# Performance work log

Hardware: AMD Instinct MI355X
Metric: run time of the kernel (lower is better)

The kernel has to match this reference:

```python
import jax, jax.numpy as jnp
import numpy as np
from jax import lax

B, C, H, Wd = 8, 3, 256, 256
K = 32           # kernels
LAT = K * 8      # 256, latent dim
P = 7            # patch size
HALF = P // 2
S = 1024         # samples per image
PD = C * P * P   # 147
NEG = 0.01       # LeakyReLU slope
EPS = 1e-5


def setup_inputs() -> dict:
    key = jax.random.key(0)
    ks = jax.random.split(key, 20)
    x = jax.random.normal(ks[0], (B, C, H, Wd), dtype=jnp.float32)
    # patch centers must satisfy HALF <= c <= H-1-HALF (here [3, 252])
    anchors_hw = jax.random.randint(ks[1], (B, S, 2), HALF, H - HALF, dtype=jnp.int32)
    positives_hw = jax.random.randint(ks[2], (B, S, 2), HALF, H - HALF, dtype=jnp.int32)
    def w(k, shape, fan_in):
        return jax.random.normal(k, shape, dtype=jnp.float32) * (1.0 / np.sqrt(fan_in))
    inp = dict(x=x, anchors_hw=anchors_hw, positives_hw=positives_hw,
               w1=w(ks[3], (K, C, 3, 3), C * 9),        g1=jnp.ones((K,), jnp.float32),        b1=jnp.zeros((K,), jnp.float32),
               w2=w(ks[4], (2 * K, K, 3, 3), K * 9),    g2=jnp.ones((2 * K,), jnp.float32),    b2=jnp.zeros((2 * K,), jnp.float32),
               w3=w(ks[5], (4 * K, 2 * K, 3, 3), 2 * K * 9), g3=jnp.ones((4 * K,), jnp.float32), b3=jnp.zeros((4 * K,), jnp.float32),
               w4=w(ks[6], (8 * K, 4 * K, 3, 3), 4 * K * 9), g4=jnp.ones((8 * K,), jnp.float32), b4=jnp.zeros((8 * K,), jnp.float32),
               lin1_w=w(ks[7], (PD, LAT), LAT), lin1_b=jnp.zeros((PD,), jnp.float32),
               lin2_w=w(ks[8], (PD, PD), PD),   lin2_b=jnp.zeros((PD,), jnp.float32))
    return inp


def _conv(x, w):
    return lax.conv_general_dilated(x, w, (1, 1), 'SAME',
                                    dimension_numbers=('NCHW', 'OIHW', 'NCHW'))


def _bn(x, g, b):
    # training-mode BatchNorm2d: batch stats over (N,H,W)
    m = x.mean(axis=(0, 2, 3), keepdims=True)
    v = x.var(axis=(0, 2, 3), keepdims=True)
    return g[None, :, None, None] * (x - m) * lax.rsqrt(v + EPS) + b[None, :, None, None]


def _lrelu(x):
    return jnp.where(x >= 0, x, NEG * x)


def _forward(x, anchors_hw, positives_hw, w1, g1, b1, w2, g2, b2, w3, g3, b3,
             w4, g4, b4, lin1_w, lin1_b, lin2_w, lin2_b):
    feat = _lrelu(_bn(_conv(x, w1), g1, b1))
    feat = _lrelu(_bn(_conv(feat, w2), g2, b2))
    feat = _lrelu(_bn(_conv(feat, w3), g3, b3))
    feat = _lrelu(_bn(_conv(feat, w4), g4, b4))  # [B, LAT, H, W]

    fhwc = jnp.transpose(feat, (0, 2, 3, 1))  # [B,H,W,LAT]
    gather_pts = jax.vmap(lambda f, hw: f[hw[:, 0], hw[:, 1]])  # per-batch fancy gather
    W_anchors = gather_pts(fhwc, anchors_hw)      # [B,S,LAT]
    W_positives = gather_pts(fhwc, positives_hw)  # [B,S,LAT]

    def slice_one(img, hw):  # img [C,H,W], hw [2]
        return lax.dynamic_slice(img, (0, hw[0] - HALF, hw[1] - HALF), (C, P, P))
    patch_real = jax.vmap(jax.vmap(slice_one, in_axes=(None, 0)))(x, anchors_hw)  # [B,S,C,P,P]

    h = _lrelu(jnp.einsum('bsl,pl->bsp', W_anchors, lin1_w) + lin1_b)
    patch_recon = (jnp.einsum('bsp,qp->bsq', h, lin2_w) + lin2_b).reshape(x.shape[0], -1, C, P, P)
    return (feat, patch_real, patch_recon, W_anchors, W_positives)


def reference(x, anchors_hw, positives_hw, w1, g1, b1, w2, g2, b2, w3, g3, b3,
              w4, g4, b4, lin1_w, lin1_b, lin2_w, lin2_b):
    return _forward(x, anchors_hw, positives_hw, w1, g1, b1, w2, g2, b2,
                    w3, g3, b3, w4, g4, b4, lin1_w, lin1_b, lin2_w, lin2_b)
```

## Files before the change

### kernel.cpp

```cpp
#include <hip/hip_runtime.h>
#include <hip/hip_bf16.h>

typedef unsigned short u16;
typedef short bf16x8 __attribute__((ext_vector_type(8)));
typedef float f32x4 __attribute__((ext_vector_type(4)));
typedef unsigned short u16x8 __attribute__((ext_vector_type(8)));

#define PD 147

static const long OFF_PREAL = 134217728L;
static const long OFF_PRECON= 135421952L;
static const long OFF_WA    = 136626176L;
static const long OFF_WP    = 138723328L;

static const long RAW_SPLIT = 100663296L;

__device__ __forceinline__ float lrelu(float v){ return v >= 0.f ? v : 0.01f*v; }

__device__ __forceinline__ float bf2f(u16 u){
    union { unsigned int i; float f; } x; x.i = ((unsigned int)u) << 16; return x.f;
}
__device__ __forceinline__ u16 f2bf(float f){
    __hip_bfloat16 h = __float2bfloat16(f);
    return *reinterpret_cast<u16*>(&h);
}

__device__ __forceinline__ void gload16(const void* g, void* l){
    __builtin_amdgcn_global_load_lds((const __attribute__((address_space(1))) void*)g,
                                     (__attribute__((address_space(3))) void*)l, 16, 0, 0);
}

template<int CIN, int KOUT, bool SPLIT>
__global__ __launch_bounds__(512)
void conv_mfma(const u16* __restrict__ fin, const u16* __restrict__ wt,
               void* __restrict__ out_, u16* __restrict__ rawhi,
               float* __restrict__ part)
{
    constexpr int CC = CIN / 32;
    constexpr int NS3 = CC * 3;
    constexpr int NF = KOUT / 64;
    constexpr int ABYTES = 2 * 324 * 32 * 2;
    constexpr int BQ = 3 * KOUT * 4;
    constexpr int NB3 = (BQ + 511) / 512;
    constexpr int BBYTES = 2 * BQ * 16;
    constexpr int EPIB = 256 * KOUT * 2;
    constexpr int SB = (ABYTES + BBYTES) > EPIB ? (ABYTES + BBYTES) : EPIB;
    __shared__ __align__(16) char smem[SB];
    u16* As = (u16*)smem;
    u16* Bs = (u16*)(smem + ABYTES);

    const int tid = threadIdx.x;
    const int w = tid >> 6, lane = tid & 63;
    const int wm = w >> 2, wn = w & 3;
    const int tile = blockIdx.x;
    const int tx0 = (tile & 15) << 4, ty0 = (tile >> 4) << 4;
    const int b = blockIdx.y;
    const long pixbase = (long)b << 16;
    const int hi = lane >> 4;

    f32x4 acc[8][NF];
#pragma unroll
    for (int m = 0; m < 8; m++)
#pragma unroll
        for (int n = 0; n < NF; n++) acc[m][n] = (f32x4){0.f,0.f,0.f,0.f};

    for (int i = tid; i < ABYTES/16; i += 512)
        ((int4*)smem)[i] = make_int4(0,0,0,0);
    __syncthreads();

    auto stage_a_round = [&](int cc, int buf, int r){
        u16* dstbase = As + buf * (324*32);
        int q = r*512 + w*64 + lane;
        int pf = q >> 2, quarter = q & 3;
        int ly = pf / 18;
        int lx = pf - ly*18;
        int gy = ty0 + ly - 1, gx = tx0 + lx - 1;
        bool ok = (q < 1296) && ((unsigned)gy < 256u) && ((unsigned)gx < 256u);
        const u16* src = fin + ((pixbase + (gy<<8) + gx) * CIN + cc*32 + quarter*8);
        u16* dst = dstbase + (r*512 + w*64) * 8;
        if (ok) gload16(src, dst);
    };
    auto stage_b3 = [&](int s, int buf){
        int cc = s / 3, dyr = s - cc*3;
        int t0 = dyr * 3;
        u16* dstbase = Bs + buf * (BQ*16/2);
#pragma unroll
        for (int r = 0; r < NB3; ++r){
            int q = r*512 + w*64 + lane;
            int tl = q / (KOUT*4);
            int qq = q - tl*(KOUT*4);
            int k = qq >> 2, quarter = qq & 3;
            const u16* src = wt + (((long)(t0+tl)*KOUT + k) * CIN + cc*32 + quarter*8);
            u16* dst = dstbase + (r*512 + w*64) * 8;
            if (q < BQ) gload16(src, dst);
        }
    };

    stage_a_round(0, 0, 0); stage_a_round(0, 0, 1); stage_a_round(0, 0, 2);
    stage_b3(0, 0);
    __syncthreads();

#pragma unroll 1
    for (int s = 0; s < NS3; ++s){
        int cc = s / 3, dyr = s - cc*3;
        if (s + 1 < NS3) stage_b3(s + 1, (s + 1) & 1);
        if (cc + 1 < CC) stage_a_round(cc + 1, (cc + 1) & 1, dyr);

        const u16* Ab = As + (cc & 1) * (324*32);
        const u16* Bb = Bs + (s & 1) * (BQ*16/2);
#pragma unroll
        for (int t = 0; t < 3; ++t){
            bf16x8 av[8];
#pragma unroll
            for (int m = 0; m < 8; m++){
                int pf = (wm*8 + m + dyr)*18 + (lane & 15) + t;
                av[m] = *(const bf16x8*)(Ab + pf*32 + hi*8);
            }
            bf16x8 bv[NF];
#pragma unroll
            for (int n = 0; n < NF; n++){
                int ch = (wn*NF + n)*16 + (lane & 15);
                bv[n] = *(const bf16x8*)(Bb + (t*KOUT + ch)*32 + hi*8);
            }
#pragma unroll
            for (int m = 0; m < 8; m++)
#pragma unroll
                for (int n = 0; n < NF; n++)
                    acc[m][n] = __builtin_amdgcn_mfma_f32_16x16x32_bf16(av[m], bv[n], acc[m][n], 0, 0, 0);
        }
        __syncthreads();
    }

    {
        const int bid = blockIdx.y * 256 + blockIdx.x;
        const long slot = (long)bid * 2 + wm;
#pragma unroll
        for (int n = 0; n < NF; n++){
            float s = 0.f, s2 = 0.f;
#pragma unroll
            for (int m = 0; m < 8; m++)
#pragma unroll
                for (int j = 0; j < 4; j++){
                    float v = acc[m][n][j];
                    s += v; s2 += v*v;
                }
            s += __shfl_down(s, 32); s2 += __shfl_down(s2, 32);
            s += __shfl_down(s, 16); s2 += __shfl_down(s2, 16);
            if (lane < 16){
                int ch = (wn*NF + n)*16 + lane;
                long off = (slot*KOUT + ch)*2;
                part[off]   = s;
                part[off+1] = s2;
            }
        }
    }

    {
        u16* ep = (u16*)smem;
        u16* outh = (u16*)out_;
        if (SPLIT && b >= 6) outh = rawhi - RAW_SPLIT;
#pragma unroll
        for (int m = 0; m < 8; m++)
#pragma unroll
            for (int n = 0; n < NF; n++){
                int ch = (wn*NF + n)*16 + (lane&15);
#pragma unroll
                for (int j = 0; j < 4; j++){
                    int px = wm*128 + m*16 + (lane>>4)*4 + j;
                    ep[px*KOUT + ch] = f2bf(acc[m][n][j]);
                }
            }
        __syncthreads();
        const int n16 = 256*KOUT/8;
        const int upr = KOUT*2;
        for (int i = tid; i < n16; i += 512){
            int py = i / upr;
            int rem = i - py*upr;
            long ga = (pixbase + ((ty0+py)<<8) + tx0) * KOUT + (long)rem*8;
            *(int4*)(outh + ga) = *(int4*)(ep + (long)i*8);
        }
    }
}

__global__ __launch_bounds__(256)
void conv1_direct(const float* __restrict__ x, const float* __restrict__ w1, u16* __restrict__ f1)
{
    __shared__ float wl[864];
    const int t = threadIdx.x;
    for (int i = t; i < 864; i += 256) wl[i] = w1[i];
    __syncthreads();
    const int y = blockIdx.x, b = blockIdx.y;
    float acc[32];
#pragma unroll
    for (int k = 0; k < 32; k++) acc[k] = 0.f;
    const long ib = (long)b*3*65536;
    for (int c = 0; c < 3; c++){
#pragma unroll
        for (int dy = 0; dy < 3; dy++){
            int gy = y + dy - 1;
#pragma unroll
            for (int dx = 0; dx < 3; dx++){
                int gx = t + dx - 1;
                float v = 0.f;
                if ((unsigned)gy < 256u && (unsigned)gx < 256u)
                    v = x[ib + c*65536 + (gy<<8) + gx];
                const float* wp = &wl[c*9 + dy*3 + dx];
#pragma unroll
                for (int k = 0; k < 32; k++) acc[k] += v * wp[k*27];
            }
        }
    }
    u16 ub[32];
#pragma unroll
    for (int k = 0; k < 32; k++) ub[k] = f2bf(acc[k]);
    u16* dst = f1 + ((long)(b*65536 + (y<<8) + t)) * 32;
#pragma unroll
    for (int j = 0; j < 4; j++) *(int4*)(dst + j*8) = *(int4*)(ub + j*8);
}

__global__ __launch_bounds__(256)
void prep_w(const float* __restrict__ w, u16* __restrict__ wt, int K, int C)
{
    int i = blockIdx.x*256 + threadIdx.x;
    if (i >= 9*K*C) return;
    int c = i % C; int r = i / C; int k = r % K; int tap = r / K;
    wt[i] = f2bf(w[((long)k*C + c)*9 + tap]);
}

template<int C>
__global__ __launch_bounds__(256)
void bn_stats_nhwc(const u16* __restrict__ f, float* __restrict__ part)
{
    constexpr int CQ = C/4;
    constexpr int SUBS = 256/CQ;
    const int t = threadIdx.x;
    const int cq = t & (CQ-1);
    const int sub = t / CQ;
    const long rowbase = (long)blockIdx.x * 512;
    float s[4] = {0,0,0,0}, q2[4] = {0,0,0,0};
    for (int r = sub; r < 512; r += SUBS){
        ushort4 v = *(const ushort4*)(f + (rowbase + r)*C + cq*4);
        float x0 = bf2f(v.x), x1 = bf2f(v.y), x2 = bf2f(v.z), x3 = bf2f(v.w);
        s[0]+=x0; q2[0]+=x0*x0; s[1]+=x1; q2[1]+=x1*x1;
        s[2]+=x2; q2[2]+=x2*x2; s[3]+=x3; q2[3]+=x3*x3;
    }
    __shared__ float r0[256], r1[256];
    for (int j = 0; j < 4; j++){
        r0[t] = s[j]; r1[t] = q2[j];
        __syncthreads();
        for (int st = 128; st >= CQ; st >>= 1){
            if (t < st){ r0[t] += r0[t+st]; r1[t] += r1[t+st]; }
            __syncthreads();
        }
        if (t < CQ){
            part[((long)blockIdx.x * C + t*4 + j)*2]     = r0[t];
            part[((long)blockIdx.x * C + t*4 + j)*2 + 1] = r1[t];
        }
        __syncthreads();
    }
}

__global__ __launch_bounds__(256)
void bn_stats_final2(const float* __restrict__ part, const float* __restrict__ g,
                     const float* __restrict__ bb, int C, int NB2, float* __restrict__ ss)
{
    const int c = blockIdx.x, t = threadIdx.x;
    float s = 0.f, s2 = 0.f;
    for (int i = t; i < NB2; i += 256){
        s  += part[((long)i*C + c)*2];
        s2 += part[((long)i*C + c)*2 + 1];
    }
    __shared__ float r0[256], r1[256];
    r0[t] = s; r1[t] = s2;
    __syncthreads();
    for (int st = 128; st > 0; st >>= 1){
        if (t < st){ r0[t] += r0[t+st]; r1[t] += r1[t+st]; }
        __syncthreads();
    }
    if (t == 0){
        const float invN = 1.f/524288.f;
        float m = r0[0]*invN;
        float v = r1[0]*invN - m*m;
        float sc = g[c]/sqrtf(v + 1e-5f);
        ss[c] = sc; ss[C+c] = bb[c] - m*sc;
    }
}

template<int C>
__global__ __launch_bounds__(256)
void bn_apply(u16* __restrict__ f, const float* __restrict__ ss, long n8)
{
    long i = (long)blockIdx.x*256 + threadIdx.x;
    if (i >= n8) return;
    u16x8 v = *(u16x8*)(f + i*8);
    int c0 = (int)((i*8) & (C-1));
#pragma unroll
    for (int j = 0; j < 8; j++){
        float xx = bf2f(v[j]);
        xx = lrelu(ss[c0+j]*xx + ss[C+c0+j]);
        v[j] = f2bf(xx);
    }
    *(u16x8*)(f + i*8) = v;
}

__global__ __launch_bounds__(256)
void bn_expand_t(const u16* __restrict__ rawlo, const u16* __restrict__ rawhi,
                 const float* __restrict__ ss, float* __restrict__ feat, int b0)
{
    __shared__ u16 lds[64*258];
    const int bid = blockIdx.x;
    const int b = b0 + (bid >> 10);
    const int px0 = (bid & 1023) * 64;
    const long p0 = (((long)(b<<16) + px0)) << 8;
    const u16* src = (b < 6) ? (rawlo + p0) : (rawhi + (p0 - RAW_SPLIT));
    const int t = threadIdx.x;
#pragma unroll
    for (int it = 0; it < 8; ++it){
        int i = it*256 + t;
        int px = i >> 5, u = i & 31;
        *(u16x8*)&lds[px*258 + u*8] = *(const u16x8*)(src + (long)i*8);
    }
    __syncthreads();
#pragma unroll
    for (int it = 0; it < 16; ++it){
        int idx = it*256 + t;
        int ch = idx >> 4;
        int q  = idx & 15;
        const float sc = ss[ch], sh = ss[256 + ch];
        float4 o;
        o.x = lrelu(sc*bf2f(lds[(q*4+0)*258 + ch]) + sh);
        o.y = lrelu(sc*bf2f(lds[(q*4+1)*258 + ch]) + sh);
        o.z = lrelu(sc*bf2f(lds[(q*4+2)*258 + ch]) + sh);
        o.w = lrelu(sc*bf2f(lds[(q*4+3)*258 + ch]) + sh);
        *(float4*)(feat + (((long)(b*256 + ch)) << 16) + px0 + q*4) = o;
    }
}

__global__ __launch_bounds__(256)
void gather_w_raw(const u16* __restrict__ rawlo, const u16* __restrict__ rawhi,
                  const float* __restrict__ ss, const int* __restrict__ hw,
                  float* __restrict__ outW)
{
    const int site = blockIdx.x;
    const int b = site >> 10;
    const int y = hw[site*2], x = hw[site*2 + 1];
    const int c = threadIdx.x;
    const long p = ((long)((b<<16) + (y<<8) + x)) << 8;
    const u16* base = (b < 6) ? (rawlo + p) : (rawhi + (p - RAW_SPLIT));
    float v = bf2f(base[c]);
    outW[(long)site*256 + c] = lrelu(ss[c]*v + ss[256 + c]);
}

__global__ __launch_bounds__(256)
void gather_patch(const float* __restrict__ x, const int* __restrict__ hw,
                  float* __restrict__ out)
{
    const long i = (long)blockIdx.x*256 + threadIdx.x;
    if (i >= 1204224L) return;
    const int px = (int)(i % 7);
    long r = i / 7;
    const int py = (int)(r % 7); r /= 7;
    const int c  = (int)(r % 3); r /= 3;
    const int s  = (int)(r % 1024);
    const int b  = (int)(r / 1024);
    const int site = b*1024 + s;
    const int yy = hw[site*2]     - 3 + py;
    const int xx = hw[site*2 + 1] - 3 + px;
    out[i] = x[(((long)(b*3 + c)) << 16) + ((long)yy << 8) + xx];
}

__global__ __launch_bounds__(256)
void mlp8(const float* __restrict__ Wa, const float* __restrict__ l1w,
          const float* __restrict__ l1b, const float* __restrict__ l2w,
          const float* __restrict__ l2b, float* __restrict__ out)
{
    __shared__ float wa[2048];
    __shared__ float h[8][152];
    const int blk = blockIdx.x;
    const int t = threadIdx.x;
#pragma unroll
    for (int it = 0; it < 8; ++it)
        wa[it*256 + t] = Wa[(long)blk*2048 + it*256 + t];
    __syncthreads();
    if (t < PD){
        float a[8] = {0,0,0,0,0,0,0,0};
        const float* wr = l1w + t*256;
#pragma unroll 4
        for (int l = 0; l < 256; ++l){
            float wv = wr[l];
#pragma unroll
            for (int g = 0; g < 8; ++g) a[g] += wa[g*256 + l]*wv;
        }
        float bb = l1b[t];
#pragma unroll
        for (int g = 0; g < 8; ++g) h[g][t] = lrelu(a[g] + bb);
    }
    __syncthreads();
    if (t < PD){
        float r[8] = {0,0,0,0,0,0,0,0};
        const float* wr = l2w + t*PD;
        for (int p = 0; p < PD; ++p){
            float wv = wr[p];
#pragma unroll
            for (int g = 0; g < 8; ++g) r[g] += h[g][p]*wv;
        }
        float bb = l2b[t];
#pragma unroll
        for (int g = 0; g < 8; ++g)
            out[((long)(blk*8 + g))*PD + t] = r[g] + bb;
    }
}

extern "C" void kernel_launch(void* const* d_in, const int* in_sizes, int n_in,
                              void* d_out, int out_size, void* d_ws, size_t ws_size,
                              hipStream_t stream)
{
    const float* x   = (const float*)d_in[0];
    const int*   anc = (const int*)  d_in[1];
    const int*   pos = (const int*)  d_in[2];
    const float* w1  = (const float*)d_in[3];
    const float* g1  = (const float*)d_in[4];
    const float* b1  = (const float*)d_in[5];
    const float* w2  = (const float*)d_in[6];
    const float* g2  = (const float*)d_in[7];
    const float* b2  = (const float*)d_in[8];
    const float* w3  = (const float*)d_in[9];
    const float* g3  = (const float*)d_in[10];
    const float* b3  = (const float*)d_in[11];
    const float* w4  = (const float*)d_in[12];
    const float* g4  = (const float*)d_in[13];
    const float* b4  = (const float*)d_in[14];
    const float* l1w = (const float*)d_in[15];
    const float* l1b = (const float*)d_in[16];
    const float* l2w = (const float*)d_in[17];
    const float* l2b = (const float*)d_in[18];

    float* feat = (float*)d_out;
    float* oPR  = feat + OFF_PREAL;
    float* oRC  = feat + OFF_PRECON;
    float* oWA  = feat + OFF_WA;
    float* oWP  = feat + OFF_WP;

    char* wsb = (char*)d_ws;
    u16* f2b = (u16*)wsb;
    u16* f3b = (u16*)(wsb + 67108864L);
    u16* f1b = (u16*)(wsb + 134217728L);

    u16* rawlo = (u16*)d_out + 167772160L;
    u16* rawhi = f2b;

    u16* Wt2 = (u16*)oWA;
    u16* Wt3 = Wt2 + 18432;
    u16* Wt4 = Wt3 + 73728;
    float* part = oWP;
    float* ss1 = oRC, *ss2 = oRC + 64, *ss3 = oRC + 192, *ss4 = oRC + 448;

    prep_w<<<72,   256, 0, stream>>>(w2, Wt2, 64, 32);
    prep_w<<<288,  256, 0, stream>>>(w3, Wt3, 128, 64);
    prep_w<<<1152, 256, 0, stream>>>(w4, Wt4, 256, 128);

    conv1_direct<<<dim3(256,8), 256, 0, stream>>>(x, w1, f1b);
    bn_stats_nhwc<32><<<1024, 256, 0, stream>>>(f1b, part);
    bn_stats_final2<<<32, 256, 0, stream>>>(part, g1, b1, 32, 1024, ss1);
    bn_apply<32><<<8192, 256, 0, stream>>>(f1b, ss1, 2097152L);

    conv_mfma<32,64,false><<<dim3(256,8), 512, 0, stream>>>(f1b, Wt2, f2b, nullptr, part);
    bn_stats_final2<<<64, 256, 0, stream>>>(part, g2, b2, 64, 4096, ss2);
    bn_apply<64><<<16384, 256, 0, stream>>>(f2b, ss2, 4194304L);

    conv_mfma<64,128,false><<<dim3(256,8), 512, 0, stream>>>(f2b, Wt3, f3b, nullptr, part);
    bn_stats_final2<<<128, 256, 0, stream>>>(part, g3, b3, 128, 4096, ss3);
    bn_apply<128><<<32768, 256, 0, stream>>>(f3b, ss3, 8388608L);

    conv_mfma<128,256,true><<<dim3(256,8), 512, 0, stream>>>(f3b, Wt4, rawlo, rawhi, part);
    bn_stats_final2<<<256, 256, 0, stream>>>(part, g4, b4, 256, 4096, ss4);

    gather_w_raw<<<8192, 256, 0, stream>>>(rawlo, rawhi, ss4, anc, oWA);
    gather_w_raw<<<8192, 256, 0, stream>>>(rawlo, rawhi, ss4, pos, oWP);
    gather_patch<<<4704, 256, 0, stream>>>(x, anc, oPR);

    bn_expand_t<<<5120, 256, 0, stream>>>(rawlo, rawhi, ss4, feat, 0);
    bn_expand_t<<<1024, 256, 0, stream>>>(rawlo, rawhi, ss4, feat, 5);
    bn_expand_t<<<2048, 256, 0, stream>>>(rawlo, rawhi, ss4, feat, 6);

    mlp8<<<1024, 256, 0, stream>>>(oWA, l1w, l1b, l2w, l2b, oRC);
}
```

Before: 824.0 us.

## Fuse BN-apply and LeakyReLU into next conv's input staging

Removes the separate bn_apply passes over layers 1-3 and instead applies scale/shift plus LeakyReLU while staging input tiles into LDS inside the conv kernel. This saves a full read-modify-write of each intermediate activation tensor. In exchange, the A-tile staging moves from asynchronous global-to-LDS loads to synchronous register loads with per-element math, and halo elements are recomputed by neighbouring tiles. Zero padding is now written explicitly instead of relying on a one-time LDS clear.

```diff
diff --git a/kernel.cpp b/kernel.cpp
--- a/kernel.cpp
+++ b/kernel.cpp
@@ -33,6 +33,7 @@
 template<int CIN, int KOUT, bool SPLIT>
 __global__ __launch_bounds__(512)
 void conv_mfma(const u16* __restrict__ fin, const u16* __restrict__ wt,
+               const float* __restrict__ ssin,
                void* __restrict__ out_, u16* __restrict__ rawhi,
                float* __restrict__ part)
 {
@@ -57,6 +58,7 @@
     const int b = blockIdx.y;
     const long pixbase = (long)b << 16;
     const int hi = lane >> 4;
+    const int quarter = lane & 3;
 
     f32x4 acc[8][NF];
 #pragma unroll
@@ -64,21 +66,31 @@
 #pragma unroll
         for (int n = 0; n < NF; n++) acc[m][n] = (f32x4){0.f,0.f,0.f,0.f};
 
-    for (int i = tid; i < ABYTES/16; i += 512)
-        ((int4*)smem)[i] = make_int4(0,0,0,0);
-    __syncthreads();
+    float sc8[8], sh8[8];
+    auto load_ss = [&](int cc){
+        int c0 = cc*32 + quarter*8;
+#pragma unroll
+        for (int j = 0; j < 8; j++){
+            sc8[j] = ssin[c0 + j];
+            sh8[j] = ssin[CIN + c0 + j];
+        }
+    };
 
     auto stage_a_round = [&](int cc, int buf, int r){
-        u16* dstbase = As + buf * (324*32);
         int q = r*512 + w*64 + lane;
-        int pf = q >> 2, quarter = q & 3;
-        int ly = pf / 18;
-        int lx = pf - ly*18;
+        int pf = q >> 2;
+        int ly = pf / 18, lx = pf - ly*18;
         int gy = ty0 + ly - 1, gx = tx0 + lx - 1;
         bool ok = (q < 1296) && ((unsigned)gy < 256u) && ((unsigned)gx < 256u);
-        const u16* src = fin + ((pixbase + (gy<<8) + gx) * CIN + cc*32 + quarter*8);
-        u16* dst = dstbase + (r*512 + w*64) * 8;
-        if (ok) gload16(src, dst);
+        u16x8 o = (u16x8){0,0,0,0,0,0,0,0};
+        if (ok){
+            u16x8 v = *(const u16x8*)(fin + ((pixbase + (gy<<8) + gx) * CIN + cc*32 + quarter*8));
+#pragma unroll
+            for (int j = 0; j < 8; j++)
+                o[j] = f2bf(lrelu(sc8[j]*bf2f(v[j]) + sh8[j]));
+        }
+        if (q < 1296)
+            *(u16x8*)(As + buf*(324*32) + q*8) = o;
     };
     auto stage_b3 = [&](int s, int buf){
         int cc = s / 3, dyr = s - cc*3;
@@ -89,13 +101,14 @@
             int q = r*512 + w*64 + lane;
             int tl = q / (KOUT*4);
             int qq = q - tl*(KOUT*4);
-            int k = qq >> 2, quarter = qq & 3;
-            const u16* src = wt + (((long)(t0+tl)*KOUT + k) * CIN + cc*32 + quarter*8);
+            int k = qq >> 2, bq = qq & 3;
+            const u16* src = wt + (((long)(t0+tl)*KOUT + k) * CIN + cc*32 + bq*8);
             u16* dst = dstbase + (r*512 + w*64) * 8;
             if (q < BQ) gload16(src, dst);
         }
     };
 
+    load_ss(0);
     stage_a_round(0, 0, 0); stage_a_round(0, 0, 1); stage_a_round(0, 0, 2);
     stage_b3(0, 0);
     __syncthreads();
@@ -104,7 +117,10 @@
     for (int s = 0; s < NS3; ++s){
         int cc = s / 3, dyr = s - cc*3;
         if (s + 1 < NS3) stage_b3(s + 1, (s + 1) & 1);
-        if (cc + 1 < CC) stage_a_round(cc + 1, (cc + 1) & 1, dyr);
+        if (cc + 1 < CC){
+            if (dyr == 0) load_ss(cc + 1);
+            stage_a_round(cc + 1, (cc + 1) & 1, dyr);
+        }
 
         const u16* Ab = As + (cc & 1) * (324*32);
         const u16* Bb = Bs + (s & 1) * (BQ*16/2);
@@ -284,23 +300,6 @@
         float sc = g[c]/sqrtf(v + 1e-5f);
         ss[c] = sc; ss[C+c] = bb[c] - m*sc;
     }
-}
-
-template<int C>
-__global__ __launch_bounds__(256)
-void bn_apply(u16* __restrict__ f, const float* __restrict__ ss, long n8)
-{
-    long i = (long)blockIdx.x*256 + threadIdx.x;
-    if (i >= n8) return;
-    u16x8 v = *(u16x8*)(f + i*8);
-    int c0 = (int)((i*8) & (C-1));
-#pragma unroll
-    for (int j = 0; j < 8; j++){
-        float xx = bf2f(v[j]);
-        xx = lrelu(ss[c0+j]*xx + ss[C+c0+j]);
-        v[j] = f2bf(xx);
-    }
-    *(u16x8*)(f + i*8) = v;
 }
 
 __global__ __launch_bounds__(256)
@@ -462,17 +461,14 @@
     conv1_direct<<<dim3(256,8), 256, 0, stream>>>(x, w1, f1b);
     bn_stats_nhwc<32><<<1024, 256, 0, stream>>>(f1b, part);
     bn_stats_final2<<<32, 256, 0, stream>>>(part, g1, b1, 32, 1024, ss1);
-    bn_apply<32><<<8192, 256, 0, stream>>>(f1b, ss1, 2097152L);
-
-    conv_mfma<32,64,false><<<dim3(256,8), 512, 0, stream>>>(f1b, Wt2, f2b, nullptr, part);
+
+    conv_mfma<32,64,false><<<dim3(256,8), 512, 0, stream>>>(f1b, Wt2, ss1, f2b, nullptr, part);
     bn_stats_final2<<<64, 256, 0, stream>>>(part, g2, b2, 64, 4096, ss2);
-    bn_apply<64><<<16384, 256, 0, stream>>>(f2b, ss2, 4194304L);
-
-    conv_mfma<64,128,false><<<dim3(256,8), 512, 0, stream>>>(f2b, Wt3, f3b, nullptr, part);
+
+    conv_mfma<64,128,false><<<dim3(256,8), 512, 0, stream>>>(f2b, Wt3, ss2, f3b, nullptr, part);
     bn_stats_final2<<<128, 256, 0, stream>>>(part, g3, b3, 128, 4096, ss3);
-    bn_apply<128><<<32768, 256, 0, stream>>>(f3b, ss3, 8388608L);
-
-    conv_mfma<128,256,true><<<dim3(256,8), 512, 0, stream>>>(f3b, Wt4, rawlo, rawhi, part);
+
+    conv_mfma<128,256,true><<<dim3(256,8), 512, 0, stream>>>(f3b, Wt4, ss3, rawlo, rawhi, part);
     bn_stats_final2<<<256, 256, 0, stream>>>(part, g4, b4, 256, 4096, ss4);
 
     gather_w_raw<<<8192, 256, 0, stream>>>(rawlo, rawhi, ss4, anc, oWA);
```

Measured after the change: 803.3 us. 2.5% less time.
